# Kernel optimization log

Hardware: AMD Instinct MI355X
Metric: run time of the kernel (lower is better)

Reference implementation:

```python
import jax, jax.numpy as jnp
import numpy as np

N = 200000
D = 256
B = 512  # fixed num_segments (batch.max()+1 in the torch code)
LN_EPS = 1e-5


def _layernorm(h, gamma, beta):
    mu = jnp.mean(h, axis=-1, keepdims=True)
    var = jnp.var(h, axis=-1, keepdims=True)
    return (h - mu) * jax.lax.rsqrt(var + LN_EPS) * gamma + beta


def setup_inputs() -> dict:
    key = jax.random.key(0)
    ks = jax.random.split(key, 10)
    x = jax.random.normal(ks[0], (N, D), dtype=jnp.float32)
    batch = jnp.sort(jax.random.randint(ks[1], (N,), 0, B)).astype(jnp.int64)
    s = 0.05
    return {
        "x": x,
        "batch": batch,
        "vn_embed": jax.random.normal(ks[2], (1, D), dtype=jnp.float32) * 0.02,
        "W1": jax.random.normal(ks[3], (D, D), dtype=jnp.float32) * s,
        "b1": jnp.zeros((D,), dtype=jnp.float32),
        "g1": jnp.ones((D,), dtype=jnp.float32),
        "be1": jnp.zeros((D,), dtype=jnp.float32),
        "W2": jax.random.normal(ks[4], (D, D), dtype=jnp.float32) * s,
        "b2": jnp.zeros((D,), dtype=jnp.float32),
        "g2": jnp.ones((D,), dtype=jnp.float32),
        "be2": jnp.zeros((D,), dtype=jnp.float32),
        "Wg": jax.random.normal(ks[5], (2 * D, D), dtype=jnp.float32) * s,
        "bg": jnp.zeros((D,), dtype=jnp.float32),
    }


def reference(x, batch, vn_embed, W1, b1, g1, be1, W2, b2, g2, be2, Wg, bg):
    # scatter-mean: per-graph average of node features  [B, D]
    seg_sum = jax.ops.segment_sum(x, batch, num_segments=B)
    cnt = jax.ops.segment_sum(jnp.ones((x.shape[0],), x.dtype), batch, num_segments=B)
    node_agg = seg_sum / jnp.maximum(cnt, 1.0)[:, None]
    # node_to_vn: Linear + GELU(exact) + LayerNorm (dropout = identity at eval)
    vn_update = _layernorm(jax.nn.gelu(node_agg @ W1 + b1, approximate=False), g1, be1)
    vn_state = vn_embed + vn_update  # vn_embed broadcasts [1,D] -> [B,D]
    # gather broadcast back to nodes + vn_to_node MLP
    vn_broadcast = vn_state[batch]  # [N, D]
    node_update = _layernorm(jax.nn.gelu(vn_broadcast @ W2 + b2, approximate=False), g2, be2)
    # sigmoid gate on concat + gated residual
    gate = jax.nn.sigmoid(jnp.concatenate([x, node_update], axis=-1) @ Wg + bg)
    x_out = x + gate * node_update
    return (x_out, vn_state)
```

## Files before the change

kernel.cpp:

```cpp
#include <hip/hip_runtime.h>
#include <hip/hip_bf16.h>
#include <math.h>

#define DIM 256
#define B_SEG 512
#define LN_EPS 1e-5f

typedef __attribute__((ext_vector_type(8))) short bf16x8;
typedef __attribute__((ext_vector_type(4))) float f32x4;

__device__ __forceinline__ float gelu_exact(float v) {
    return 0.5f * v * (1.0f + erff(v * 0.70710678118654752f));
}

__device__ __forceinline__ unsigned int pack2bf(float a, float b) {
    unsigned int ua = (unsigned int)__bfloat16_as_ushort(__float2bfloat16(a));
    unsigned int ub = (unsigned int)__bfloat16_as_ushort(__float2bfloat16(b));
    return ua | (ub << 16);
}

__device__ __forceinline__ void async16(const void* g, void* l) {
    __builtin_amdgcn_global_load_lds(
        (const __attribute__((address_space(1))) void*)(g),
        (__attribute__((address_space(3))) void*)(l), 16, 0, 0);
}

__global__ __launch_bounds__(256) void k_prep(const float* __restrict__ Wg,
                                              __hip_bfloat16* __restrict__ Wt2,
                                              const int* __restrict__ batch,
                                              int* __restrict__ seg_start,
                                              float* __restrict__ extra, int n) {
    if (blockIdx.x < 256) {
        int k = blockIdx.x;
        int c = threadIdx.x;
        Wt2[((size_t)(k >> 3) << 11) + (c << 3) + (k & 7)] = __float2bfloat16(Wg[(size_t)k * DIM + c]);
        return;
    }
    if (blockIdx.x == 256) {
        for (int s = threadIdx.x; s <= B_SEG; s += 256) {
            int lo = 0, hi = n;
            while (lo < hi) {
                int mid = (lo + hi) >> 1;
                if (batch[mid] < s) lo = mid + 1; else hi = mid;
            }
            seg_start[s] = lo;
        }
        return;
    }
    int b = blockIdx.x - 257;
    ((float4*)extra)[(size_t)b * 256 + threadIdx.x] = make_float4(0.f, 0.f, 0.f, 0.f);
}

__global__ __launch_bounds__(256, 2) void k_pass1(const float* __restrict__ x,
                                                  const int* __restrict__ batch,
                                                  float* __restrict__ part,
                                                  unsigned int* __restrict__ hdr,
                                                  float* __restrict__ extra,
                                                  __hip_bfloat16* __restrict__ xbf,
                                                  int n, int emit) {
    __shared__ __align__(16) char sX[64 * 1024];

    const int tile = blockIdx.x;
    const int i0   = tile * 64;
    if (i0 >= n) return;
    const int iN   = min(i0 + 64, n);

    const int tid  = threadIdx.x;
    const int wave = tid >> 6;
    const int lane = tid & 63;

    if (iN - i0 == 64) {
        const char* gsrc = (const char*)x + (size_t)i0 * 1024;
        #pragma unroll
        for (int j = 0; j < 16; ++j)
            async16(gsrc + j * 4096 + tid * 16, sX + j * 4096 + wave * 1024);
    } else {
        for (int v = tid; v < 64 * 64; v += 256) {
            int r = v >> 6, c = v & 63;
            float4 val = (i0 + r < n) ? *(const float4*)(x + (size_t)(i0 + r) * DIM + c * 4)
                                      : make_float4(0.f, 0.f, 0.f, 0.f);
            *(float4*)(sX + r * 1024 + c * 16) = val;
        }
    }
    __syncthreads();

    const int sf = batch[i0];
    const int sl = batch[iN - 1];

    float4 accA = make_float4(0.f, 0.f, 0.f, 0.f);
    float4 accB = make_float4(0.f, 0.f, 0.f, 0.f);

    const int rbase = wave * 16;
    #pragma unroll
    for (int jj = 0; jj < 16; ++jj) {
        const int r  = rbase + jj;
        const int gr = i0 + r;
        const bool valid = gr < n;
        float4 v = *(const float4*)(sX + r * 1024 + lane * 16);
        int b = valid ? batch[gr] : -2;
        if (emit && valid) {
            uint2 pk;
            pk.x = pack2bf(v.x, v.y);
            pk.y = pack2bf(v.z, v.w);
            *(uint2*)((char*)xbf + (size_t)gr * 512 + ((lane * 8) ^ ((r & 7) << 4))) = pk;
        }
        if (b == sf) {
            accA.x += v.x; accA.y += v.y; accA.z += v.z; accA.w += v.w;
        } else if (b == sl) {
            accB.x += v.x; accB.y += v.y; accB.z += v.z; accB.w += v.w;
        } else if (valid) {
            atomicAdd(&extra[(size_t)b * DIM + lane * 4 + 0], v.x);
            atomicAdd(&extra[(size_t)b * DIM + lane * 4 + 1], v.y);
            atomicAdd(&extra[(size_t)b * DIM + lane * 4 + 2], v.z);
            atomicAdd(&extra[(size_t)b * DIM + lane * 4 + 3], v.w);
        }
    }

    __syncthreads();
    float4* red = (float4*)sX;
    red[(wave * 2 + 0) * 64 + lane] = accA;
    red[(wave * 2 + 1) * 64 + lane] = accB;
    __syncthreads();
    if (wave == 0) {
        float4 a0 = red[0 * 64 + lane], a1 = red[2 * 64 + lane],
               a2 = red[4 * 64 + lane], a3 = red[6 * 64 + lane];
        float4 t;
        t.x = (a0.x + a1.x) + (a2.x + a3.x);
        t.y = (a0.y + a1.y) + (a2.y + a3.y);
        t.z = (a0.z + a1.z) + (a2.z + a3.z);
        t.w = (a0.w + a1.w) + (a2.w + a3.w);
        *(float4*)(part + ((size_t)tile * 2 + 0) * DIM + lane * 4) = t;
        if (lane == 0) hdr[tile] = (unsigned int)sf | ((unsigned int)sl << 16);
    } else if (wave == 1) {
        float4 a0 = red[1 * 64 + lane], a1 = red[3 * 64 + lane],
               a2 = red[5 * 64 + lane], a3 = red[7 * 64 + lane];
        float4 t;
        t.x = (a0.x + a1.x) + (a2.x + a3.x);
        t.y = (a0.y + a1.y) + (a2.y + a3.y);
        t.z = (a0.z + a1.z) + (a2.z + a3.z);
        t.w = (a0.w + a1.w) + (a2.w + a3.w);
        *(float4*)(part + ((size_t)tile * 2 + 1) * DIM + lane * 4) = t;
    }
}

__global__ __launch_bounds__(256) void k_vn(const float* __restrict__ part,
                                            const unsigned int* __restrict__ hdr,
                                            const float* __restrict__ extra,
                                            const int* __restrict__ seg_start,
                                            const float* __restrict__ vn_embed,
                                            const float* __restrict__ W1, const float* __restrict__ b1,
                                            const float* __restrict__ g1, const float* __restrict__ be1,
                                            const float* __restrict__ W2, const float* __restrict__ b2,
                                            const float* __restrict__ g2, const float* __restrict__ be2,
                                            const float* __restrict__ Wg, const float* __restrict__ bg,
                                            float* __restrict__ vn_state_out,
                                            float* __restrict__ nu,
                                            float* __restrict__ gpart,
                                            int use_parts) {
    __shared__ float sIn[DIM];
    __shared__ float sRed[DIM];
    __shared__ float sRed2[DIM];
    const int b = blockIdx.x;
    const int d = threadIdx.x;

    const int s0 = seg_start[b], s1 = seg_start[b + 1];
    float sum = extra[(size_t)b * DIM + d];
    if (use_parts && s1 > s0) {
        int t0 = s0 >> 6, t1 = (s1 - 1) >> 6;
        for (int t = t0; t <= t1; ++t) {
            unsigned int h = hdr[t];
            int f = (int)(h & 0xffffu), l = (int)(h >> 16);
            if (f == b) sum += part[((size_t)t * 2 + 0) * DIM + d];
            if (l == b && l != f) sum += part[((size_t)t * 2 + 1) * DIM + d];
        }
    }
    float denom = fmaxf((float)(s1 - s0), 1.0f);
    sIn[d] = sum / denom;
    __syncthreads();

    float h0 = 0.f, h1 = 0.f, h2a = 0.f, h3 = 0.f;
    for (int k = 0; k < DIM; k += 4) {
        h0  = fmaf(sIn[k + 0], W1[(size_t)(k + 0) * DIM + d], h0);
        h1  = fmaf(sIn[k + 1], W1[(size_t)(k + 1) * DIM + d], h1);
        h2a = fmaf(sIn[k + 2], W1[(size_t)(k + 2) * DIM + d], h2a);
        h3  = fmaf(sIn[k + 3], W1[(size_t)(k + 3) * DIM + d], h3);
    }
    float h = gelu_exact(b1[d] + ((h0 + h1) + (h2a + h3)));

    sRed[d] = h; sRed2[d] = h * h;
    __syncthreads();
    for (int s = 128; s > 0; s >>= 1) {
        if (d < s) { sRed[d] += sRed[d + s]; sRed2[d] += sRed2[d + s]; }
        __syncthreads();
    }
    float mu = sRed[0] * (1.0f / DIM);
    float var = fmaxf(sRed2[0] * (1.0f / DIM) - mu * mu, 0.0f);
    float rs = rsqrtf(var + LN_EPS);
    float vnst = vn_embed[d] + ((h - mu) * rs * g1[d] + be1[d]);
    vn_state_out[(size_t)b * DIM + d] = vnst;
    __syncthreads();
    sIn[d] = vnst;
    __syncthreads();

    float g0 = 0.f, g1a = 0.f, g2a = 0.f, g3 = 0.f;
    for (int k = 0; k < DIM; k += 4) {
        g0  = fmaf(sIn[k + 0], W2[(size_t)(k + 0) * DIM + d], g0);
        g1a = fmaf(sIn[k + 1], W2[(size_t)(k + 1) * DIM + d], g1a);
        g2a = fmaf(sIn[k + 2], W2[(size_t)(k + 2) * DIM + d], g2a);
        g3  = fmaf(sIn[k + 3], W2[(size_t)(k + 3) * DIM + d], g3);
    }
    float h2 = gelu_exact(b2[d] + ((g0 + g1a) + (g2a + g3)));

    sRed[d] = h2; sRed2[d] = h2 * h2;
    __syncthreads();
    for (int s = 128; s > 0; s >>= 1) {
        if (d < s) { sRed[d] += sRed[d + s]; sRed2[d] += sRed2[d + s]; }
        __syncthreads();
    }
    float mu2 = sRed[0] * (1.0f / DIM);
    float var2 = fmaxf(sRed2[0] * (1.0f / DIM) - mu2 * mu2, 0.0f);
    float rs2 = rsqrtf(var2 + LN_EPS);
    float nud = (h2 - mu2) * rs2 * g2[d] + be2[d];
    nu[(size_t)b * DIM + d] = nud;
    __syncthreads();
    sIn[d] = nud;
    __syncthreads();

    float p0 = 0.f, p1 = 0.f, p2 = 0.f, p3 = 0.f;
    for (int k = 0; k < DIM; k += 4) {
        p0 = fmaf(sIn[k + 0], Wg[(size_t)(DIM + k + 0) * DIM + d], p0);
        p1 = fmaf(sIn[k + 1], Wg[(size_t)(DIM + k + 1) * DIM + d], p1);
        p2 = fmaf(sIn[k + 2], Wg[(size_t)(DIM + k + 2) * DIM + d], p2);
        p3 = fmaf(sIn[k + 3], Wg[(size_t)(DIM + k + 3) * DIM + d], p3);
    }
    gpart[(size_t)b * DIM + d] = bg[d] + ((p0 + p1) + (p2 + p3));
}

__global__ __launch_bounds__(256, 4) void k_gate_bf(const __hip_bfloat16* __restrict__ xbf,
                                                    const int* __restrict__ batch,
                                                    const __hip_bfloat16* __restrict__ Wt2,
                                                    const float* __restrict__ nu,
                                                    const float* __restrict__ gpart,
                                                    float* __restrict__ xout,
                                                    int n) {
    __shared__ __align__(16) char sA[64 * 512];

    const int tid  = threadIdx.x;
    const int wave = tid >> 6;
    const int lane = tid & 63;
    const int r15  = lane & 15;
    const int kq   = lane >> 4;
    const size_t i0 = (size_t)blockIdx.x * 64;

    const char* gsrc = (const char*)xbf + i0 * 512;
    #pragma unroll
    for (int j = 0; j < 8; ++j)
        async16(gsrc + j * 4096 + tid * 16, sA + j * 4096 + wave * 1024);
    __syncthreads();

    f32x4 acc[4][4];
    #pragma unroll
    for (int m = 0; m < 4; ++m)
        #pragma unroll
        for (int nn = 0; nn < 4; ++nn)
            acc[m][nn] = (f32x4){0.f, 0.f, 0.f, 0.f};

    #pragma unroll
    for (int ks = 0; ks < 8; ++ks) {
        bf16x8 a[4], b[4];
        #pragma unroll
        for (int nn = 0; nn < 4; ++nn) {
            int c = wave * 64 + nn * 16 + r15;
            b[nn] = *(const bf16x8*)(Wt2 + ((size_t)(ks * 4 + kq) << 11) + (c << 3));
        }
        #pragma unroll
        for (int m = 0; m < 4; ++m) {
            int r = m * 16 + r15;
            a[m] = *(const bf16x8*)(sA + r * 512 + ((ks * 64 + kq * 16) ^ ((r & 7) << 4)));
        }
        #pragma unroll
        for (int m = 0; m < 4; ++m)
            #pragma unroll
            for (int nn = 0; nn < 4; ++nn)
                acc[m][nn] = __builtin_amdgcn_mfma_f32_16x16x32_bf16(a[m], b[nn], acc[m][nn], 0, 0, 0);
    }

    #pragma unroll
    for (int m = 0; m < 4; ++m) {
        #pragma unroll
        for (int q = 0; q < 4; ++q) {
            int rr = m * 16 + kq * 4 + q;
            long node = (long)(i0 + rr);
            if (node >= n) continue;
            int bb = batch[node];
            #pragma unroll
            for (int nn = 0; nn < 4; ++nn) {
                int col = wave * 64 + nn * 16 + r15;
                float pre = acc[m][nn][q] + gpart[bb * DIM + col];
                float e = __expf(-pre);
                float gte = __builtin_amdgcn_rcpf(1.0f + e);
                float xres = __bfloat162float(
                    *(const __hip_bfloat16*)(sA + rr * 512 + ((2 * col) ^ ((rr & 7) << 4))));
                xout[(size_t)node * DIM + col] = xres + gte * nu[bb * DIM + col];
            }
        }
    }
}

__global__ __launch_bounds__(256) void k_segsum_fp(const float* __restrict__ x,
                                                   const int* __restrict__ batch,
                                                   float* __restrict__ sums,
                                                   int n) {
    const int i0 = blockIdx.x * 64;
    if (i0 >= n) return;
    const int t    = threadIdx.x;
    const int lane = t & 63;
    const int d4   = lane * 4;
    const int rg   = t >> 6;
    float4 acc = make_float4(0.f, 0.f, 0.f, 0.f);
    int cur = -1;
    for (int j = 0; j < 16; ++j) {
        int i = i0 + rg + 4 * j;
        if (i >= n) break;
        int b = batch[i];
        if (b != cur) {
            if (cur >= 0) {
                atomicAdd(&sums[(size_t)cur * DIM + d4 + 0], acc.x);
                atomicAdd(&sums[(size_t)cur * DIM + d4 + 1], acc.y);
                atomicAdd(&sums[(size_t)cur * DIM + d4 + 2], acc.z);
                atomicAdd(&sums[(size_t)cur * DIM + d4 + 3], acc.w);
            }
            acc = make_float4(0.f, 0.f, 0.f, 0.f);
            cur = b;
        }
        float4 v = *(const float4*)(x + (size_t)i * DIM + d4);
        acc.x += v.x; acc.y += v.y; acc.z += v.z; acc.w += v.w;
    }
    if (cur >= 0) {
        atomicAdd(&sums[(size_t)cur * DIM + d4 + 0], acc.x);
        atomicAdd(&sums[(size_t)cur * DIM + d4 + 1], acc.y);
        atomicAdd(&sums[(size_t)cur * DIM + d4 + 2], acc.z);
        atomicAdd(&sums[(size_t)cur * DIM + d4 + 3], acc.w);
    }
}

__global__ __launch_bounds__(256) void k_gate_fp(const float* __restrict__ x,
                                                 const int* __restrict__ batch,
                                                 const __hip_bfloat16* __restrict__ Wt2,
                                                 const float* __restrict__ nu,
                                                 const float* __restrict__ gpart,
                                                 float* __restrict__ xout,
                                                 int n) {
    __shared__ __align__(16) char sA[32 * 512];
    const int tid  = threadIdx.x;
    const int wave = tid >> 6;
    const int lane = tid & 63;
    const int r15  = lane & 15;
    const int kq   = lane >> 4;
    const int i0   = blockIdx.x * 32;

    float4 av0[4], av1[4];
    #pragma unroll
    for (int j = 0; j < 4; ++j) {
        int v = j * 256 + tid;
        int r = v >> 5;
        int k8 = v & 31;
        int node = i0 + r;
        if (node < n) {
            const float* p = x + (size_t)node * DIM + k8 * 8;
            av0[j] = *(const float4*)p;
            av1[j] = *(const float4*)(p + 4);
        } else {
            av0[j] = make_float4(0.f, 0.f, 0.f, 0.f);
            av1[j] = av0[j];
        }
    }
    #pragma unroll
    for (int j = 0; j < 4; ++j) {
        int v = j * 256 + tid;
        int r = v >> 5;
        int k8 = v & 31;
        uint4 pk;
        pk.x = pack2bf(av0[j].x, av0[j].y);
        pk.y = pack2bf(av0[j].z, av0[j].w);
        pk.z = pack2bf(av1[j].x, av1[j].y);
        pk.w = pack2bf(av1[j].z, av1[j].w);
        *(uint4*)(sA + r * 512 + ((k8 * 16) ^ ((r & 7) << 4))) = pk;
    }
    __syncthreads();

    f32x4 acc[2][4];
    #pragma unroll
    for (int m = 0; m < 2; ++m)
        #pragma unroll
        for (int nn = 0; nn < 4; ++nn)
            acc[m][nn] = (f32x4){0.f, 0.f, 0.f, 0.f};

    #pragma unroll
    for (int ks = 0; ks < 8; ++ks) {
        bf16x8 a[2], b[4];
        #pragma unroll
        for (int nn = 0; nn < 4; ++nn) {
            int c = wave * 64 + nn * 16 + r15;
            b[nn] = *(const bf16x8*)(Wt2 + ((size_t)(ks * 4 + kq) << 11) + (c << 3));
        }
        #pragma unroll
        for (int m = 0; m < 2; ++m) {
            int r = m * 16 + r15;
            a[m] = *(const bf16x8*)(sA + r * 512 + ((ks * 64 + kq * 16) ^ ((r & 7) << 4)));
        }
        #pragma unroll
        for (int m = 0; m < 2; ++m)
            #pragma unroll
            for (int nn = 0; nn < 4; ++nn)
                acc[m][nn] = __builtin_amdgcn_mfma_f32_16x16x32_bf16(a[m], b[nn], acc[m][nn], 0, 0, 0);
    }

    #pragma unroll
    for (int m = 0; m < 2; ++m) {
        #pragma unroll
        for (int q = 0; q < 4; ++q) {
            int rr = m * 16 + kq * 4 + q;
            int node = i0 + rr;
            if (node >= n) continue;
            int bb = batch[node];
            #pragma unroll
            for (int nn = 0; nn < 4; ++nn) {
                int col = wave * 64 + nn * 16 + r15;
                float pre = acc[m][nn][q] + gpart[bb * DIM + col];
                float e = __expf(-pre);
                float gte = __builtin_amdgcn_rcpf(1.0f + e);
                float xres = __bfloat162float(
                    *(const __hip_bfloat16*)(sA + rr * 512 + ((2 * col) ^ ((rr & 7) << 4))));
                xout[(size_t)node * DIM + col] = xres + gte * nu[bb * DIM + col];
            }
        }
    }
}

extern "C" void kernel_launch(void* const* d_in, const int* in_sizes, int n_in,
                              void* d_out, int out_size, void* d_ws, size_t ws_size,
                              hipStream_t stream) {
    const float* x        = (const float*)d_in[0];
    const int*   batch    = (const int*)d_in[1];
    const float* vn_embed = (const float*)d_in[2];
    const float* W1  = (const float*)d_in[3];
    const float* b1  = (const float*)d_in[4];
    const float* g1  = (const float*)d_in[5];
    const float* be1 = (const float*)d_in[6];
    const float* W2  = (const float*)d_in[7];
    const float* b2  = (const float*)d_in[8];
    const float* g2  = (const float*)d_in[9];
    const float* be2 = (const float*)d_in[10];
    const float* Wg  = (const float*)d_in[11];
    const float* bg  = (const float*)d_in[12];

    const int n = in_sizes[0] / DIM;
    const int nt64 = (n + 63) / 64;

    float* out = (float*)d_out;
    float* xout = out;
    float* vn_state_out = out + (size_t)n * DIM;

    char* wsb = (char*)d_ws;
    int*          seg_start = (int*)wsb;
    unsigned int* hdr       = (unsigned int*)(wsb + 4096);
    float*        extra     = (float*)(wsb + 20480);
    float*        part      = (float*)(wsb + 544768);
    char*         after     = wsb + 544768 + (size_t)nt64 * 2 * DIM * 4;
    float* nu    = (float*)after;
    float* gpart = nu + (size_t)B_SEG * DIM;
    __hip_bfloat16* Wt2 = (__hip_bfloat16*)(gpart + (size_t)B_SEG * DIM);
    __hip_bfloat16* xbf = Wt2 + (size_t)DIM * DIM;

    const size_t xbf_off = (size_t)((char*)xbf - wsb);
    const size_t need = xbf_off + (size_t)nt64 * 64 * 512;
    const bool use_bf = (ws_size >= need);

    k_prep<<<385, 256, 0, stream>>>(Wg, Wt2, batch, seg_start, extra, n);

    if (use_bf) {
        k_pass1<<<nt64, 256, 0, stream>>>(x, batch, part, hdr, extra, xbf, n, 1);
    } else {
        k_segsum_fp<<<nt64, 256, 0, stream>>>(x, batch, extra, n);
    }

    k_vn<<<B_SEG, 256, 0, stream>>>(part, hdr, extra, seg_start, vn_embed,
                                    W1, b1, g1, be1,
                                    W2, b2, g2, be2,
                                    Wg, bg,
                                    vn_state_out, nu, gpart,
                                    use_bf ? 1 : 0);

    if (use_bf) {
        k_gate_bf<<<nt64, 256, 0, stream>>>(xbf, batch, Wt2, nu, gpart, xout, n);
    } else {
        int nblk3 = (n + 31) / 32;
        k_gate_fp<<<nblk3, 256, 0, stream>>>(x, batch, Wt2, nu, gpart, xout, n);
    }
}
```

Measured before the change: 204.2 us.

## Shrink pass1 tiles to 32 rows and simplify segment partial bookkeeping

The segment-sum pass now processes 32-row tiles with 32 KB of LDS and launch bounds of 4 blocks per CU instead of 64-row tiles at 2. Each half-wave handles one row with 8 contiguous floats per lane, and the bf16 copy of x is written as 16-byte stores. The first segment's partial goes to a single per-tile slot, and the last segment's partial is atomically added into extra. This removes the header array, and k_vn just sums the tile slots whose start row falls in its segment. The aim is more parallelism and occupancy plus cheaper reduction in k_vn, at the cost of more blocks and more atomics on extra.

After: 194.1 us, median of 2. 1.05x faster.

```diff
diff --git a/kernel.cpp b/kernel.cpp
--- a/kernel.cpp
+++ b/kernel.cpp
@@ -51,100 +51,123 @@
     ((float4*)extra)[(size_t)b * 256 + threadIdx.x] = make_float4(0.f, 0.f, 0.f, 0.f);
 }
 
-__global__ __launch_bounds__(256, 2) void k_pass1(const float* __restrict__ x,
+__global__ __launch_bounds__(256, 4) void k_pass1(const float* __restrict__ x,
                                                   const int* __restrict__ batch,
                                                   float* __restrict__ part,
-                                                  unsigned int* __restrict__ hdr,
                                                   float* __restrict__ extra,
                                                   __hip_bfloat16* __restrict__ xbf,
-                                                  int n, int emit) {
-    __shared__ __align__(16) char sX[64 * 1024];
+                                                  int n) {
+    __shared__ __align__(16) char sX[32 * 1024];
+    __shared__ float4 red[4][32][2];
 
     const int tile = blockIdx.x;
-    const int i0   = tile * 64;
+    const int i0   = tile * 32;
     if (i0 >= n) return;
-    const int iN   = min(i0 + 64, n);
+    const int iN   = min(i0 + 32, n);
 
     const int tid  = threadIdx.x;
     const int wave = tid >> 6;
     const int lane = tid & 63;
-
-    if (iN - i0 == 64) {
-        const char* gsrc = (const char*)x + (size_t)i0 * 1024;
-        #pragma unroll
-        for (int j = 0; j < 16; ++j)
-            async16(gsrc + j * 4096 + tid * 16, sX + j * 4096 + wave * 1024);
+    const int li   = lane & 31;
+    const int sub  = lane >> 5;
+
+    if (iN - i0 == 32) {
+        const char* g = (const char*)x + (size_t)i0 * 1024;
+        #pragma unroll
+        for (int j = 0; j < 8; ++j)
+            async16(g + j * 4096 + tid * 16, sX + j * 4096 + wave * 1024);
     } else {
-        for (int v = tid; v < 64 * 64; v += 256) {
+        for (int v = tid; v < 32 * 64; v += 256) {
             int r = v >> 6, c = v & 63;
-            float4 val = (i0 + r < n) ? *(const float4*)(x + (size_t)(i0 + r) * DIM + c * 4)
+            float4 val = (i0 + r < n) ? ((const float4*)(x + (size_t)(i0 + r) * DIM))[c]
                                       : make_float4(0.f, 0.f, 0.f, 0.f);
             *(float4*)(sX + r * 1024 + c * 16) = val;
         }
     }
-    __syncthreads();
-
     const int sf = batch[i0];
     const int sl = batch[iN - 1];
-
-    float4 accA = make_float4(0.f, 0.f, 0.f, 0.f);
-    float4 accB = make_float4(0.f, 0.f, 0.f, 0.f);
-
-    const int rbase = wave * 16;
-    #pragma unroll
-    for (int jj = 0; jj < 16; ++jj) {
-        const int r  = rbase + jj;
+    int bt[4];
+    #pragma unroll
+    for (int jj = 0; jj < 4; ++jj) {
+        int gr = i0 + wave * 8 + jj * 2 + sub;
+        bt[jj] = (gr < n) ? batch[gr] : -2;
+    }
+    __syncthreads();
+
+    float4 a0 = make_float4(0.f,0.f,0.f,0.f), a1 = a0, b0 = a0, b1 = a0;
+    #pragma unroll
+    for (int jj = 0; jj < 4; ++jj) {
+        const int r  = wave * 8 + jj * 2 + sub;
         const int gr = i0 + r;
-        const bool valid = gr < n;
-        float4 v = *(const float4*)(sX + r * 1024 + lane * 16);
-        int b = valid ? batch[gr] : -2;
-        if (emit && valid) {
-            uint2 pk;
-            pk.x = pack2bf(v.x, v.y);
-            pk.y = pack2bf(v.z, v.w);
-            *(uint2*)((char*)xbf + (size_t)gr * 512 + ((lane * 8) ^ ((r & 7) << 4))) = pk;
-        }
+        float4 v0 = *(const float4*)(sX + r * 1024 + li * 32);
+        float4 v1 = *(const float4*)(sX + r * 1024 + li * 32 + 16);
+        if (gr < n) {
+            uint4 pk;
+            pk.x = pack2bf(v0.x, v0.y); pk.y = pack2bf(v0.z, v0.w);
+            pk.z = pack2bf(v1.x, v1.y); pk.w = pack2bf(v1.z, v1.w);
+            *(uint4*)((char*)xbf + (size_t)gr * 512 + ((li * 16) ^ ((r & 7) << 4))) = pk;
+        }
+        const int b = bt[jj];
         if (b == sf) {
-            accA.x += v.x; accA.y += v.y; accA.z += v.z; accA.w += v.w;
+            a0.x += v0.x; a0.y += v0.y; a0.z += v0.z; a0.w += v0.w;
+            a1.x += v1.x; a1.y += v1.y; a1.z += v1.z; a1.w += v1.w;
         } else if (b == sl) {
-            accB.x += v.x; accB.y += v.y; accB.z += v.z; accB.w += v.w;
-        } else if (valid) {
-            atomicAdd(&extra[(size_t)b * DIM + lane * 4 + 0], v.x);
-            atomicAdd(&extra[(size_t)b * DIM + lane * 4 + 1], v.y);
-            atomicAdd(&extra[(size_t)b * DIM + lane * 4 + 2], v.z);
-            atomicAdd(&extra[(size_t)b * DIM + lane * 4 + 3], v.w);
-        }
-    }
-
-    __syncthreads();
-    float4* red = (float4*)sX;
-    red[(wave * 2 + 0) * 64 + lane] = accA;
-    red[(wave * 2 + 1) * 64 + lane] = accB;
-    __syncthreads();
-    if (wave == 0) {
-        float4 a0 = red[0 * 64 + lane], a1 = red[2 * 64 + lane],
-               a2 = red[4 * 64 + lane], a3 = red[6 * 64 + lane];
-        float4 t;
-        t.x = (a0.x + a1.x) + (a2.x + a3.x);
-        t.y = (a0.y + a1.y) + (a2.y + a3.y);
-        t.z = (a0.z + a1.z) + (a2.z + a3.z);
-        t.w = (a0.w + a1.w) + (a2.w + a3.w);
-        *(float4*)(part + ((size_t)tile * 2 + 0) * DIM + lane * 4) = t;
-        if (lane == 0) hdr[tile] = (unsigned int)sf | ((unsigned int)sl << 16);
-    } else if (wave == 1) {
-        float4 a0 = red[1 * 64 + lane], a1 = red[3 * 64 + lane],
-               a2 = red[5 * 64 + lane], a3 = red[7 * 64 + lane];
-        float4 t;
-        t.x = (a0.x + a1.x) + (a2.x + a3.x);
-        t.y = (a0.y + a1.y) + (a2.y + a3.y);
-        t.z = (a0.z + a1.z) + (a2.z + a3.z);
-        t.w = (a0.w + a1.w) + (a2.w + a3.w);
-        *(float4*)(part + ((size_t)tile * 2 + 1) * DIM + lane * 4) = t;
+            b0.x += v0.x; b0.y += v0.y; b0.z += v0.z; b0.w += v0.w;
+            b1.x += v1.x; b1.y += v1.y; b1.z += v1.z; b1.w += v1.w;
+        } else if (gr < n) {
+            float* e = &extra[(size_t)b * DIM + li * 8];
+            atomicAdd(e + 0, v0.x); atomicAdd(e + 1, v0.y);
+            atomicAdd(e + 2, v0.z); atomicAdd(e + 3, v0.w);
+            atomicAdd(e + 4, v1.x); atomicAdd(e + 5, v1.y);
+            atomicAdd(e + 6, v1.z); atomicAdd(e + 7, v1.w);
+        }
+    }
+
+    a0.x += __shfl_xor(a0.x, 32); a0.y += __shfl_xor(a0.y, 32);
+    a0.z += __shfl_xor(a0.z, 32); a0.w += __shfl_xor(a0.w, 32);
+    a1.x += __shfl_xor(a1.x, 32); a1.y += __shfl_xor(a1.y, 32);
+    a1.z += __shfl_xor(a1.z, 32); a1.w += __shfl_xor(a1.w, 32);
+
+    if (sub == 0) { red[wave][li][0] = a0; red[wave][li][1] = a1; }
+    __syncthreads();
+    if (wave == 0 && sub == 0) {
+        #pragma unroll
+        for (int half = 0; half < 2; ++half) {
+            float4 r0 = red[0][li][half], r1 = red[1][li][half],
+                   r2 = red[2][li][half], r3 = red[3][li][half];
+            float4 t;
+            t.x = (r0.x + r1.x) + (r2.x + r3.x);
+            t.y = (r0.y + r1.y) + (r2.y + r3.y);
+            t.z = (r0.z + r1.z) + (r2.z + r3.z);
+            t.w = (r0.w + r1.w) + (r2.w + r3.w);
+            *(float4*)(part + (size_t)tile * DIM + li * 8 + half * 4) = t;
+        }
+    }
+
+    if (sf != sl) {
+        b0.x += __shfl_xor(b0.x, 32); b0.y += __shfl_xor(b0.y, 32);
+        b0.z += __shfl_xor(b0.z, 32); b0.w += __shfl_xor(b0.w, 32);
+        b1.x += __shfl_xor(b1.x, 32); b1.y += __shfl_xor(b1.y, 32);
+        b1.z += __shfl_xor(b1.z, 32); b1.w += __shfl_xor(b1.w, 32);
+        __syncthreads();
+        if (sub == 0) { red[wave][li][0] = b0; red[wave][li][1] = b1; }
+        __syncthreads();
+        if (wave == 0 && sub == 0) {
+            float* e = &extra[(size_t)sl * DIM + li * 8];
+            #pragma unroll
+            for (int half = 0; half < 2; ++half) {
+                float4 r0 = red[0][li][half], r1 = red[1][li][half],
+                       r2 = red[2][li][half], r3 = red[3][li][half];
+                atomicAdd(e + half * 4 + 0, (r0.x + r1.x) + (r2.x + r3.x));
+                atomicAdd(e + half * 4 + 1, (r0.y + r1.y) + (r2.y + r3.y));
+                atomicAdd(e + half * 4 + 2, (r0.z + r1.z) + (r2.z + r3.z));
+                atomicAdd(e + half * 4 + 3, (r0.w + r1.w) + (r2.w + r3.w));
+            }
+        }
     }
 }
 
 __global__ __launch_bounds__(256) void k_vn(const float* __restrict__ part,
-                                            const unsigned int* __restrict__ hdr,
                                             const float* __restrict__ extra,
                                             const int* __restrict__ seg_start,
                                             const float* __restrict__ vn_embed,
@@ -165,14 +188,9 @@
 
     const int s0 = seg_start[b], s1 = seg_start[b + 1];
     float sum = extra[(size_t)b * DIM + d];
-    if (use_parts && s1 > s0) {
-        int t0 = s0 >> 6, t1 = (s1 - 1) >> 6;
-        for (int t = t0; t <= t1; ++t) {
-            unsigned int h = hdr[t];
-            int f = (int)(h & 0xffffu), l = (int)(h >> 16);
-            if (f == b) sum += part[((size_t)t * 2 + 0) * DIM + d];
-            if (l == b && l != f) sum += part[((size_t)t * 2 + 1) * DIM + d];
-        }
+    if (use_parts) {
+        const int t0 = (s0 + 31) >> 5, t1 = (s1 + 31) >> 5;
+        for (int t = t0; t < t1; ++t) sum += part[(size_t)t * DIM + d];
     }
     float denom = fmaxf((float)(s1 - s0), 1.0f);
     sIn[d] = sum / denom;
@@ -456,6 +474,7 @@
     const float* bg  = (const float*)d_in[12];
 
     const int n = in_sizes[0] / DIM;
+    const int nt32 = (n + 31) / 32;
     const int nt64 = (n + 63) / 64;
 
     float* out = (float*)d_out;
@@ -463,11 +482,10 @@
     float* vn_state_out = out + (size_t)n * DIM;
 
     char* wsb = (char*)d_ws;
-    int*          seg_start = (int*)wsb;
-    unsigned int* hdr       = (unsigned int*)(wsb + 4096);
-    float*        extra     = (float*)(wsb + 20480);
-    float*        part      = (float*)(wsb + 544768);
-    char*         after     = wsb + 544768 + (size_t)nt64 * 2 * DIM * 4;
+    int*   seg_start = (int*)wsb;
+    float* extra     = (float*)(wsb + 4096);
+    float* part      = (float*)(wsb + 4096 + 524288);
+    char*  after     = wsb + 4096 + 524288 + (size_t)nt32 * DIM * 4;
     float* nu    = (float*)after;
     float* gpart = nu + (size_t)B_SEG * DIM;
     __hip_bfloat16* Wt2 = (__hip_bfloat16*)(gpart + (size_t)B_SEG * DIM);
@@ -480,12 +498,12 @@
     k_prep<<<385, 256, 0, stream>>>(Wg, Wt2, batch, seg_start, extra, n);
 
     if (use_bf) {
-        k_pass1<<<nt64, 256, 0, stream>>>(x, batch, part, hdr, extra, xbf, n, 1);
+        k_pass1<<<nt32, 256, 0, stream>>>(x, batch, part, extra, xbf, n);
     } else {
         k_segsum_fp<<<nt64, 256, 0, stream>>>(x, batch, extra, n);
     }
 
-    k_vn<<<B_SEG, 256, 0, stream>>>(part, hdr, extra, seg_start, vn_embed,
+    k_vn<<<B_SEG, 256, 0, stream>>>(part, extra, seg_start, vn_embed,
                                     W1, b1, g1, be1,
                                     W2, b2, g2, be2,
                                     Wg, bg,
```
